# Kernel optimization log

Measured on AMD Instinct MI355X. Metric: run time of the kernel, lower is better.

Reference implementation:

```python
import jax, jax.numpy as jnp
import numpy as np

# Stochastic-computing layer: values in [0,1] are encoded as random bitstreams
# (bit = uniform <= value), multiply = AND, and the reduction over input rows is
# a chained random MUX (tf.where with p=0.5 coins), then mean over the bit axis.
BATCH, D_IN, D_OUT, BIT_SIZE = 512, 1024, 1024, 128


def setup_inputs() -> dict:
    key = jax.random.key(0)
    kx, kw = jax.random.split(key)
    # bitstream-encoded probabilities in [0, 1]
    x = jax.random.uniform(kx, (BATCH, D_IN), dtype=jnp.float32)
    w = jax.random.uniform(kw, (D_IN, D_OUT), dtype=jnp.float32)
    return {"x": x, "w": w}


def reference(x, w):
    B, Din = x.shape
    Dout = w.shape[1]
    key = jax.random.key(42)
    kx, kw, kc = jax.random.split(key, 3)

    # bitstream generation: bit = (uniform <= value)
    x_bits = jax.random.uniform(kx, (B, Din, BIT_SIZE)) <= x[:, :, None]        # (B, Din, T) bool
    w_bits = jax.random.uniform(kw, (Din, Dout, BIT_SIZE)) <= w[:, :, None]     # (Din, Dout, T) bool

    # Chained random MUX over rows 1..Din-2 (mirrors `for row in range(1, dim-1)`):
    #   final = where(coin, final, row_r)  ->  result is row r of the LAST step
    #   whose coin was False; row 0 if every coin was True. Coins are shared
    #   across the output dim (original select_line shape (B, 1, T)).
    n_steps = Din - 2
    coins = jax.random.uniform(kc, (n_steps, B, BIT_SIZE)) <= 0.5               # (steps, B, T) bool
    rows = jnp.arange(1, Din - 1)                                               # (steps,)
    idx = jnp.max(jnp.where(~coins, rows[:, None, None], 0), axis=0)            # (B, T) int

    # Gather the selected row's bits instead of materializing (B, Din, Dout, T)
    chosen_x = jnp.take_along_axis(x_bits, idx[:, None, :], axis=1)[:, 0, :]    # (B, T)
    w_bt = jnp.transpose(w_bits, (0, 2, 1))                                     # (Din, T, Dout)
    chosen_w = w_bt[idx, jnp.arange(BIT_SIZE)[None, :], :]                      # (B, T, Dout)

    # stochastic multiply (AND) then decode via mean over the bit axis
    final = (chosen_x[:, :, None] & chosen_w).astype(jnp.float32)               # (B, T, Dout)
    return jnp.mean(final, axis=1)                                              # (B, Dout)
```

## Files before the change

### kernel.cpp

```cpp
#include <hip/hip_runtime.h>
#include <stdint.h>

#define BATCH 512
#define D_IN 1024
#define D_OUT 1024
#define BITSZ 128
#define N_STEPS (D_IN - 2)

#define IBASE 960
#define ICAP 64

#define WS_V_OFF 0u
#define WS_V_BYTES (BATCH * BITSZ * 4u)
#define WS_VT_OFF (WS_V_OFF + WS_V_BYTES)
#define WS_VT_BYTES (BITSZ * BATCH * 4u)
#define WS_TAB_OFF (WS_VT_OFF + WS_VT_BYTES)
#define WS_TAB_BYTES (BITSZ * ICAP * 32u * 4u)
#define WS_NEEDED (WS_TAB_OFF + WS_TAB_BYTES)

#define TSTRIDE 132

__host__ __device__ __forceinline__ uint32_t rotl32(uint32_t x, uint32_t d) {
  return (x << d) | (x >> (32u - d));
}

__host__ __device__ __forceinline__ void threefry2x32(uint32_t k0, uint32_t k1,
                                                      uint32_t& x0, uint32_t& x1) {
  const uint32_t k2 = k0 ^ k1 ^ 0x1BD11BDAu;
  x0 += k0; x1 += k1;
#define TFR(r) { x0 += x1; x1 = rotl32(x1, (r)); x1 ^= x0; }
  TFR(13) TFR(15) TFR(26) TFR(6)
  x0 += k1; x1 += k2 + 1u;
  TFR(17) TFR(29) TFR(16) TFR(24)
  x0 += k2; x1 += k0 + 2u;
  TFR(13) TFR(15) TFR(26) TFR(6)
  x0 += k0; x1 += k1 + 3u;
  TFR(17) TFR(29) TFR(16) TFR(24)
  x0 += k1; x1 += k2 + 4u;
  TFR(13) TFR(15) TFR(26) TFR(6)
  x0 += k2; x1 += k0 + 5u;
#undef TFR
}

__device__ __forceinline__ float runif(uint32_t k0, uint32_t k1, uint32_t n) {
  uint32_t x0 = 0u, x1 = n;
  threefry2x32(k0, k1, x0, x1);
  const uint32_t b = x0 ^ x1;
  return __uint_as_float((b >> 9) | 0x3f800000u) - 1.0f;
}

__device__ __forceinline__ int scan_idx(uint32_t bt, uint32_t ck0, uint32_t ck1) {
  int idx = 0;
  int s;
  for (s = N_STEPS - 1; s >= 3; s -= 4) {
    const float u0 = runif(ck0, ck1, ((uint32_t)(s)     << 16) + bt);
    const float u1 = runif(ck0, ck1, ((uint32_t)(s - 1) << 16) + bt);
    const float u2 = runif(ck0, ck1, ((uint32_t)(s - 2) << 16) + bt);
    const float u3 = runif(ck0, ck1, ((uint32_t)(s - 3) << 16) + bt);
    if (u0 > 0.5f) { idx = s + 1; break; }
    if (u1 > 0.5f) { idx = s;     break; }
    if (u2 > 0.5f) { idx = s - 1; break; }
    if (u3 > 0.5f) { idx = s - 2; break; }
  }
  if (idx == 0 && s < 3) {
    const float u0 = runif(ck0, ck1, (1u << 16) + bt);
    const float u1 = runif(ck0, ck1, bt);
    if (u0 > 0.5f)      idx = 2;
    else if (u1 > 0.5f) idx = 1;
  }
  return idx;
}

__global__ void __launch_bounds__(256) k_idx(const float* __restrict__ x,
                                             int* __restrict__ v,
                                             int* __restrict__ vt,
                                             uint32_t ck0, uint32_t ck1,
                                             uint32_t xk0, uint32_t xk1,
                                             int use_tab) {
  const int tid = blockIdx.x * 256 + threadIdx.x;
  const int b = tid >> 7;
  const int t = tid & 127;
  const int idx = scan_idx((uint32_t)tid, ck0, ck1);
  const float ux = runif(xk0, xk1,
      ((uint32_t)b << 17) + ((uint32_t)idx << 7) + (uint32_t)t);
  const int xb = (ux <= x[b * D_IN + idx]) ? 1 : 0;
  const int val = xb ? idx : -1;
  v[tid] = val;
  if (use_tab) vt[t * BATCH + b] = val;
}

__global__ void __launch_bounds__(1024) k_tab(const float* __restrict__ w,
                                              const int* __restrict__ vt,
                                              uint32_t* __restrict__ tab,
                                              uint32_t wk0, uint32_t wk1) {
  const int t = blockIdx.x >> 1;
  const int h = blockIdx.x & 1;
  const int tid = threadIdx.x;

  __shared__ uint32_t s_bm[2];
  __shared__ int s_rows[ICAP];
  if (tid < 2) s_bm[tid] = 0u;
  __syncthreads();

  unsigned long long m64 = 0;
  if (tid < BATCH) {
    const int code = vt[t * BATCH + tid];
    if (code >= IBASE) m64 = 1ull << (code - IBASE);
  }
  for (int off = 32; off; off >>= 1) m64 |= __shfl_down(m64, off);
  if ((tid & 63) == 0 && tid < BATCH) {
    if ((uint32_t)m64)         atomicOr(&s_bm[0], (uint32_t)m64);
    if ((uint32_t)(m64 >> 32)) atomicOr(&s_bm[1], (uint32_t)(m64 >> 32));
  }
  __syncthreads();

  const unsigned long long bm = (unsigned long long)s_bm[0] |
                                ((unsigned long long)s_bm[1] << 32);
  const int cnt = __popcll(bm);
  if (tid < 64 && ((bm >> tid) & 1ull))
    s_rows[__popcll(bm & ((1ull << tid) - 1ull))] = tid;
  __syncthreads();

  const int g = (tid < 512) ? 0 : 1;
  const int dl = (tid < 512) ? tid : (tid - 512);
  const int d = h * 512 + dl;
  const int lane = tid & 63;
  const int wbase = (d >> 5) & ~1;
  const float* wcol = w + d;
  for (int r = g; r < cnt; r += 2) {
    const int j = s_rows[r];
    const int i = IBASE + j;
    const float u = runif(wk0, wk1,
        ((uint32_t)i << 17) + ((uint32_t)d << 7) + (uint32_t)t);
    const unsigned long long mb = __ballot(u <= wcol[i * D_OUT]);
    uint32_t* row = tab + (((t << 6) + j) << 5);
    if (lane == 0)  row[wbase]     = (uint32_t)mb;
    if (lane == 32) row[wbase + 1] = (uint32_t)(mb >> 32);
  }
}

__global__ void __launch_bounds__(512) k_acc(const float* __restrict__ w,
                                             const int* __restrict__ v,
                                             const uint32_t* __restrict__ tab,
                                             float* __restrict__ out,
                                             uint32_t wk0, uint32_t wk1,
                                             int use_tab) {
  const int b = blockIdx.x;
  const int tid = threadIdx.x;

  __shared__ __align__(16) uint32_t s_tab2[32 * TSTRIDE];
  __shared__ int s_list[BITSZ];
  __shared__ int s_wcnt[2];
  __shared__ int s_anyfb;

  if (tid == 0) s_anyfb = use_tab ? 0 : 1;

  unsigned long long mb = 0;
  int code = -1;
  bool act = false;
  if (tid < BITSZ) {
    code = v[b * BITSZ + tid];
    act = code >= 0;
    mb = __ballot(act);
    if ((tid & 63) == 0) s_wcnt[tid >> 6] = __popcll(mb);
  }
  __syncthreads();
  const int m = s_wcnt[0] + s_wcnt[1];
  const int m4 = (m + 3) & ~3;
  if (tid < BITSZ && act) {
    const int lane = tid & 63;
    const int pos = ((tid >= 64) ? s_wcnt[0] : 0) +
                    __popcll(mb & ((1ull << lane) - 1ull));
    s_list[pos] = (code << 7) | tid;
    if (code < IBASE) atomicOr(&s_anyfb, 1);
  }
  __syncthreads();

  if (s_anyfb == 0) {
    const int wrd = tid & 31;
    for (int jj = tid >> 5; jj < m; jj += 16) {
      const int e = s_list[jj];
      const int i = e >> 7, t = e & 127;
      s_tab2[wrd * TSTRIDE + jj] = tab[(((t << 6) + (i - IBASE)) << 5) + wrd];
    }
    if (tid < 32)
      for (int jj = m; jj < m4; ++jj) s_tab2[tid * TSTRIDE + jj] = 0u;
    __syncthreads();

    const int dw0 = tid >> 5, db = tid & 31;
    const int dw1 = dw0 + 16;
    const uint32_t* c0 = &s_tab2[dw0 * TSTRIDE];
    const uint32_t* c1 = &s_tab2[dw1 * TSTRIDE];
    int a0 = 0, a1 = 0;
    for (int k = 0; k < m4; k += 4) {
      const uint4 r0 = *(const uint4*)(c0 + k);
      const uint4 r1 = *(const uint4*)(c1 + k);
      a0 += (r0.x >> db) & 1u; a0 += (r0.y >> db) & 1u;
      a0 += (r0.z >> db) & 1u; a0 += (r0.w >> db) & 1u;
      a1 += (r1.x >> db) & 1u; a1 += (r1.y >> db) & 1u;
      a1 += (r1.z >> db) & 1u; a1 += (r1.w >> db) & 1u;
    }
    out[b * D_OUT + tid]       = (float)a0 * (1.0f / (float)BITSZ);
    out[b * D_OUT + tid + 512] = (float)a1 * (1.0f / (float)BITSZ);
  } else {
    const int d0 = tid, d1 = tid + 512;
    int a0 = 0, a1 = 0;
    for (int jj = 0; jj < m; ++jj) {
      const int e = s_list[jj];
      const int i = e >> 7, t = e & 127;
      const float u0 = runif(wk0, wk1,
          ((uint32_t)i << 17) + ((uint32_t)d0 << 7) + (uint32_t)t);
      const float u1 = runif(wk0, wk1,
          ((uint32_t)i << 17) + ((uint32_t)d1 << 7) + (uint32_t)t);
      a0 += (u0 <= w[i * D_OUT + d0]) ? 1 : 0;
      a1 += (u1 <= w[i * D_OUT + d1]) ? 1 : 0;
    }
    out[b * D_OUT + d0] = (float)a0 * (1.0f / (float)BITSZ);
    out[b * D_OUT + d1] = (float)a1 * (1.0f / (float)BITSZ);
  }
}

struct TFKeys { uint32_t xk0, xk1, wk0, wk1, ck0, ck1; };

static TFKeys derive_keys() {
  TFKeys K;
  uint32_t a0 = 0, a1 = 0; threefry2x32(0u, 42u, a0, a1); K.xk0 = a0; K.xk1 = a1;
  uint32_t b0 = 0, b1 = 1; threefry2x32(0u, 42u, b0, b1); K.wk0 = b0; K.wk1 = b1;
  uint32_t c0 = 0, c1 = 2; threefry2x32(0u, 42u, c0, c1); K.ck0 = c0; K.ck1 = c1;
  return K;
}

extern "C" void kernel_launch(void* const* d_in, const int* in_sizes, int n_in,
                              void* d_out, int out_size, void* d_ws, size_t ws_size,
                              hipStream_t stream) {
  const float* x = (const float*)d_in[0];
  const float* w = (const float*)d_in[1];
  if (n_in >= 2 && in_sizes[0] == D_IN * D_OUT && in_sizes[1] == BATCH * D_IN) {
    const float* tmp = x; x = w; w = tmp;
  }
  float* out = (float*)d_out;
  char* ws = (char*)d_ws;
  int* v = (int*)(ws + WS_V_OFF);
  int* vt = (int*)(ws + WS_VT_OFF);
  uint32_t* tab = (uint32_t*)(ws + WS_TAB_OFF);

  const int use_tab = (ws_size >= WS_NEEDED) ? 1 : 0;
  const TFKeys K = derive_keys();

  hipLaunchKernelGGL(k_idx, dim3((BATCH * BITSZ) / 256), dim3(256), 0, stream,
                     x, v, vt, K.ck0, K.ck1, K.xk0, K.xk1, use_tab);
  if (use_tab)
    hipLaunchKernelGGL(k_tab, dim3(BITSZ * 2), dim3(1024), 0, stream,
                       w, vt, tab, K.wk0, K.wk1);
  hipLaunchKernelGGL(k_acc, dim3(BATCH), dim3(512), 0, stream,
                     w, v, tab, out, K.wk0, K.wk1, use_tab);
}
```

Baseline: 22.39 us.

## Fuse index scan into table-build kernel, dropping transposed index buffer

Merges the index-scan kernel into the table-building kernel. Each block now recomputes the MUX indices for its bit position across all batch rows, instead of reading a transposed index array written by a separate launch. This removes one kernel launch and the vt round trip through global memory. In exchange the scan work is done twice, once per half-block pair. The table loop is also unrolled by two so the weight loads and RNG calls of two rows overlap, and the fallback detection in the accumulate kernel uses a ballot instead of a shared atomic.

```diff
diff --git a/kernel.cpp b/kernel.cpp
--- a/kernel.cpp
+++ b/kernel.cpp
@@ -12,13 +12,13 @@
 
 #define WS_V_OFF 0u
 #define WS_V_BYTES (BATCH * BITSZ * 4u)
-#define WS_VT_OFF (WS_V_OFF + WS_V_BYTES)
-#define WS_VT_BYTES (BITSZ * BATCH * 4u)
-#define WS_TAB_OFF (WS_VT_OFF + WS_VT_BYTES)
+#define WS_TAB_OFF (WS_V_OFF + WS_V_BYTES)
 #define WS_TAB_BYTES (BITSZ * ICAP * 32u * 4u)
 #define WS_NEEDED (WS_TAB_OFF + WS_TAB_BYTES)
 
 #define TSTRIDE 132
+
+struct TFKeys { uint32_t xk0, xk1, wk0, wk1, ck0, ck1; };
 
 __host__ __device__ __forceinline__ uint32_t rotl32(uint32_t x, uint32_t d) {
   return (x << d) | (x >> (32u - d));
@@ -71,71 +71,64 @@
   return idx;
 }
 
-__global__ void __launch_bounds__(256) k_idx(const float* __restrict__ x,
-                                             int* __restrict__ v,
-                                             int* __restrict__ vt,
-                                             uint32_t ck0, uint32_t ck1,
-                                             uint32_t xk0, uint32_t xk1,
-                                             int use_tab) {
-  const int tid = blockIdx.x * 256 + threadIdx.x;
-  const int b = tid >> 7;
-  const int t = tid & 127;
-  const int idx = scan_idx((uint32_t)tid, ck0, ck1);
-  const float ux = runif(xk0, xk1,
-      ((uint32_t)b << 17) + ((uint32_t)idx << 7) + (uint32_t)t);
-  const int xb = (ux <= x[b * D_IN + idx]) ? 1 : 0;
-  const int val = xb ? idx : -1;
-  v[tid] = val;
-  if (use_tab) vt[t * BATCH + b] = val;
-}
-
-__global__ void __launch_bounds__(1024) k_tab(const float* __restrict__ w,
-                                              const int* __restrict__ vt,
+__global__ void __launch_bounds__(512) k_tabx(const float* __restrict__ x,
+                                              const float* __restrict__ w,
+                                              int* __restrict__ v,
                                               uint32_t* __restrict__ tab,
-                                              uint32_t wk0, uint32_t wk1) {
+                                              TFKeys K) {
   const int t = blockIdx.x >> 1;
   const int h = blockIdx.x & 1;
   const int tid = threadIdx.x;
 
-  __shared__ uint32_t s_bm[2];
+  __shared__ unsigned long long s_bmw[8];
   __shared__ int s_rows[ICAP];
-  if (tid < 2) s_bm[tid] = 0u;
-  __syncthreads();
-
-  unsigned long long m64 = 0;
-  if (tid < BATCH) {
-    const int code = vt[t * BATCH + tid];
-    if (code >= IBASE) m64 = 1ull << (code - IBASE);
-  }
-  for (int off = 32; off; off >>= 1) m64 |= __shfl_down(m64, off);
-  if ((tid & 63) == 0 && tid < BATCH) {
-    if ((uint32_t)m64)         atomicOr(&s_bm[0], (uint32_t)m64);
-    if ((uint32_t)(m64 >> 32)) atomicOr(&s_bm[1], (uint32_t)(m64 >> 32));
-  }
-  __syncthreads();
-
-  const unsigned long long bm = (unsigned long long)s_bm[0] |
-                                ((unsigned long long)s_bm[1] << 32);
+
+  const int b = tid;
+  const int idx = scan_idx(((uint32_t)b << 7) + (uint32_t)t, K.ck0, K.ck1);
+  const float ux = runif(K.xk0, K.xk1,
+      ((uint32_t)b << 17) + ((uint32_t)idx << 7) + (uint32_t)t);
+  const int xb = (ux <= x[b * D_IN + idx]) ? 1 : 0;
+  if (h == 0) v[b * BITSZ + t] = xb ? idx : -1;
+
+  unsigned long long me =
+      (xb && idx >= IBASE) ? (1ull << (idx - IBASE)) : 0ull;
+#pragma unroll
+  for (int off = 1; off < 64; off <<= 1) me |= __shfl_xor(me, off);
+  if ((tid & 63) == 0) s_bmw[tid >> 6] = me;
+  __syncthreads();
+
+  unsigned long long bm = s_bmw[0];
+#pragma unroll
+  for (int wv = 1; wv < 8; ++wv) bm |= s_bmw[wv];
   const int cnt = __popcll(bm);
   if (tid < 64 && ((bm >> tid) & 1ull))
     s_rows[__popcll(bm & ((1ull << tid) - 1ull))] = tid;
   __syncthreads();
 
-  const int g = (tid < 512) ? 0 : 1;
-  const int dl = (tid < 512) ? tid : (tid - 512);
-  const int d = h * 512 + dl;
+  const int d = h * 512 + tid;
   const int lane = tid & 63;
   const int wbase = (d >> 5) & ~1;
+  const uint32_t nbase = ((uint32_t)d << 7) + (uint32_t)t;
   const float* wcol = w + d;
-  for (int r = g; r < cnt; r += 2) {
-    const int j = s_rows[r];
-    const int i = IBASE + j;
-    const float u = runif(wk0, wk1,
-        ((uint32_t)i << 17) + ((uint32_t)d << 7) + (uint32_t)t);
-    const unsigned long long mb = __ballot(u <= wcol[i * D_OUT]);
-    uint32_t* row = tab + (((t << 6) + j) << 5);
-    if (lane == 0)  row[wbase]     = (uint32_t)mb;
-    if (lane == 32) row[wbase + 1] = (uint32_t)(mb >> 32);
+  for (int r = 0; r < cnt; r += 2) {
+    const int j0 = s_rows[r];
+    const bool have1 = (r + 1) < cnt;
+    const int j1 = have1 ? s_rows[r + 1] : j0;
+    const int i0 = IBASE + j0, i1 = IBASE + j1;
+    const float w0 = wcol[i0 * D_OUT];
+    const float w1 = wcol[i1 * D_OUT];
+    const float u0 = runif(K.wk0, K.wk1, ((uint32_t)i0 << 17) + nbase);
+    const float u1 = runif(K.wk0, K.wk1, ((uint32_t)i1 << 17) + nbase);
+    const unsigned long long m0 = __ballot(u0 <= w0);
+    uint32_t* row0 = tab + (((t << 6) + j0) << 5);
+    if (lane == 0)  row0[wbase]     = (uint32_t)m0;
+    if (lane == 32) row0[wbase + 1] = (uint32_t)(m0 >> 32);
+    if (have1) {
+      const unsigned long long m1 = __ballot(u1 <= w1);
+      uint32_t* row1 = tab + (((t << 6) + j1) << 5);
+      if (lane == 0)  row1[wbase]     = (uint32_t)m1;
+      if (lane == 32) row1[wbase + 1] = (uint32_t)(m1 >> 32);
+    }
   }
 }
 
@@ -151,9 +144,7 @@
   __shared__ __align__(16) uint32_t s_tab2[32 * TSTRIDE];
   __shared__ int s_list[BITSZ];
   __shared__ int s_wcnt[2];
-  __shared__ int s_anyfb;
-
-  if (tid == 0) s_anyfb = use_tab ? 0 : 1;
+  __shared__ uint32_t s_fb[2];
 
   unsigned long long mb = 0;
   int code = -1;
@@ -162,21 +153,25 @@
     code = v[b * BITSZ + tid];
     act = code >= 0;
     mb = __ballot(act);
-    if ((tid & 63) == 0) s_wcnt[tid >> 6] = __popcll(mb);
+    const unsigned long long fbm = __ballot(act && code < IBASE);
+    if ((tid & 63) == 0) {
+      s_wcnt[tid >> 6] = __popcll(mb);
+      s_fb[tid >> 6] = (fbm != 0ull) ? 1u : 0u;
+    }
   }
   __syncthreads();
   const int m = s_wcnt[0] + s_wcnt[1];
   const int m4 = (m + 3) & ~3;
+  const bool anyfb = (!use_tab) || (s_fb[0] | s_fb[1]);
   if (tid < BITSZ && act) {
     const int lane = tid & 63;
     const int pos = ((tid >= 64) ? s_wcnt[0] : 0) +
                     __popcll(mb & ((1ull << lane) - 1ull));
     s_list[pos] = (code << 7) | tid;
-    if (code < IBASE) atomicOr(&s_anyfb, 1);
-  }
-  __syncthreads();
-
-  if (s_anyfb == 0) {
+  }
+  __syncthreads();
+
+  if (!anyfb) {
     const int wrd = tid & 31;
     for (int jj = tid >> 5; jj < m; jj += 16) {
       const int e = s_list[jj];
@@ -188,9 +183,8 @@
     __syncthreads();
 
     const int dw0 = tid >> 5, db = tid & 31;
-    const int dw1 = dw0 + 16;
     const uint32_t* c0 = &s_tab2[dw0 * TSTRIDE];
-    const uint32_t* c1 = &s_tab2[dw1 * TSTRIDE];
+    const uint32_t* c1 = &s_tab2[(dw0 + 16) * TSTRIDE];
     int a0 = 0, a1 = 0;
     for (int k = 0; k < m4; k += 4) {
       const uint4 r0 = *(const uint4*)(c0 + k);
@@ -220,7 +214,19 @@
   }
 }
 
-struct TFKeys { uint32_t xk0, xk1, wk0, wk1, ck0, ck1; };
+__global__ void __launch_bounds__(256) k_idx(const float* __restrict__ x,
+                                             int* __restrict__ v,
+                                             uint32_t ck0, uint32_t ck1,
+                                             uint32_t xk0, uint32_t xk1) {
+  const int tid = blockIdx.x * 256 + threadIdx.x;
+  const int b = tid >> 7;
+  const int t = tid & 127;
+  const int idx = scan_idx((uint32_t)tid, ck0, ck1);
+  const float ux = runif(xk0, xk1,
+      ((uint32_t)b << 17) + ((uint32_t)idx << 7) + (uint32_t)t);
+  const int xb = (ux <= x[b * D_IN + idx]) ? 1 : 0;
+  v[tid] = xb ? idx : -1;
+}
 
 static TFKeys derive_keys() {
   TFKeys K;
@@ -241,17 +247,18 @@
   float* out = (float*)d_out;
   char* ws = (char*)d_ws;
   int* v = (int*)(ws + WS_V_OFF);
-  int* vt = (int*)(ws + WS_VT_OFF);
   uint32_t* tab = (uint32_t*)(ws + WS_TAB_OFF);
 
   const int use_tab = (ws_size >= WS_NEEDED) ? 1 : 0;
   const TFKeys K = derive_keys();
 
-  hipLaunchKernelGGL(k_idx, dim3((BATCH * BITSZ) / 256), dim3(256), 0, stream,
-                     x, v, vt, K.ck0, K.ck1, K.xk0, K.xk1, use_tab);
-  if (use_tab)
-    hipLaunchKernelGGL(k_tab, dim3(BITSZ * 2), dim3(1024), 0, stream,
-                       w, vt, tab, K.wk0, K.wk1);
+  if (use_tab) {
+    hipLaunchKernelGGL(k_tabx, dim3(BITSZ * 2), dim3(512), 0, stream,
+                       x, w, v, tab, K);
+  } else {
+    hipLaunchKernelGGL(k_idx, dim3((BATCH * BITSZ) / 256), dim3(256), 0, stream,
+                       x, v, K.ck0, K.ck1, K.xk0, K.xk1);
+  }
   hipLaunchKernelGGL(k_acc, dim3(BATCH), dim3(512), 0, stream,
                      w, v, tab, out, K.wk0, K.wk1, use_tab);
 }
```

Measured after the change: 22.82 us. About the same (+1.9%).
